# Kernel optimization log

Measured on AMD Instinct MI355X. Metric: run time of the kernel, lower is better.

The kernel has to match this reference:

```python
import jax, jax.numpy as jnp
import numpy as np

N_DOC, N_WORD, N_ENT, N_POS = 10000, 20000, 10000, 60
D, D_POS_IN, D_WEMB = 128, 60, 300
E11, E22, E33, E01, E02, E03 = 320000, 160000, 3600, 300000, 100000, 150000
EPS = 1e-9


def spmm(rows, cols, vals, x, n_out):
    """Sparse (n_out x n_in) adjacency @ x via gather + weighted segment-sum."""
    return jax.ops.segment_sum(vals[:, None] * x[cols], rows, num_segments=n_out)


def gcn(rows, cols, vals, x, n_out, W=None, b=None):
    """GCN layer: adj @ (x W + b) with ReLU; identity=True in torch == W is None."""
    h = x if W is None else x @ W + b
    return jax.nn.relu(spmm(rows, cols, vals, h, n_out))


def setup_inputs():
    key = jax.random.key(0)
    ks = iter(jax.random.split(key, 64))
    randn = lambda s: jax.random.normal(next(ks), s, jnp.float32)
    rand = lambda s: jax.random.uniform(next(ks), s, dtype=jnp.float32)
    ridx = lambda s, hi: jax.random.randint(next(ks), s, 0, hi, jnp.int32)
    return {
        "f1": randn((N_WORD, D)),
        "f2": randn((N_ENT, D)),
        "f3": randn((N_POS, D_POS_IN)),
        "word_emb": randn((N_ENT, D_WEMB)),
        "a11_rows": ridx((E11,), N_WORD), "a11_cols": ridx((E11,), N_WORD), "a11_vals": rand((E11,)),
        "a22_rows": ridx((E22,), N_ENT), "a22_cols": ridx((E22,), N_ENT), "a22_vals": rand((E22,)),
        "a33_rows": ridx((E33,), N_POS), "a33_cols": ridx((E33,), N_POS), "a33_vals": rand((E33,)),
        "a01_rows": ridx((E01,), N_DOC), "a01_cols": ridx((E01,), N_WORD), "a01_vals": rand((E01,)),
        "a02_rows": ridx((E02,), N_DOC), "a02_cols": ridx((E02,), N_ENT), "a02_vals": rand((E02,)),
        "a03_rows": ridx((E03,), N_DOC), "a03_cols": ridx((E03,), N_POS), "a03_vals": rand((E03,)),
        "W3": randn((D_POS_IN, D)) * 0.1, "b3": jnp.zeros((D,), jnp.float32),
        "W1_2": randn((D, D)) * 0.1, "b1_2": jnp.zeros((D,), jnp.float32),
        "W2_2": randn((D, D)) * 0.1, "b2_2": jnp.zeros((D,), jnp.float32),
        "W3_2": randn((D, D)) * 0.1, "b3_2": jnp.zeros((D,), jnp.float32),
    }


def reference(f1, f2, f3, word_emb,
              a11_rows, a11_cols, a11_vals, a22_rows, a22_cols, a22_vals,
              a33_rows, a33_cols, a33_vals, a01_rows, a01_cols, a01_vals,
              a02_rows, a02_cols, a02_vals, a03_rows, a03_cols, a03_vals,
              W3, b3, W1_2, b1_2, W2_2, b2_2, W3_2, b3_2):
    # eval mode: F.dropout(training=False) is a no-op
    # type 1 (words): GCN(identity=True) -> GCN_2
    h1 = gcn(a11_rows, a11_cols, a11_vals, f1, N_WORD)
    h1 = gcn(a11_rows, a11_cols, a11_vals, h1, N_WORD, W1_2, b1_2)
    # type 2 (entities, concat_word_emb=True): GCN(identity=True) -> GCN_2 -> concat word_emb
    h2 = gcn(a22_rows, a22_cols, a22_vals, f2, N_ENT)
    h2 = gcn(a22_rows, a22_cols, a22_vals, h2, N_ENT, W2_2, b2_2)
    h2 = jnp.concatenate([h2, word_emb], axis=-1)  # [N_ENT, D + D_WEMB]
    # type 3 (POS): full GCN -> GCN_2
    h3 = gcn(a33_rows, a33_cols, a33_vals, f3, N_POS, W3, b3)
    h3 = gcn(a33_rows, a33_cols, a33_vals, h3, N_POS, W3_2, b3_2)
    # cross-type aggregation onto documents + L2 normalization
    outs = []
    for rows, cols, vals, h in ((a01_rows, a01_cols, a01_vals, h1),
                                (a02_rows, a02_cols, a02_vals, h2),
                                (a03_rows, a03_cols, a03_vals, h3)):
        agg = spmm(rows, cols, vals, h, N_DOC)  # [N_DOC, d]
        outs.append(agg / (jnp.linalg.norm(agg, axis=-1, keepdims=True) + EPS))
    return tuple(outs)
```

## Files before the change

kernel.cpp:

```cpp
#include <hip/hip_runtime.h>
#include <hip/hip_bf16.h>

typedef __hip_bfloat16 bf16;

#define N_DOC   10000
#define N_WORD  20000
#define N_ENT   10000
#define N_POS   60
#define DD      128
#define D_WEMB  300
#define E11     320000
#define E22     160000
#define E33     3600
#define E01     300000
#define E02     100000
#define E03     150000

#define ROFF11  0
#define ROFF22  20000
#define ROFF33  30000
#define ROFF01  30060
#define ROFF02  40060
#define ROFF03  50060
#define NROWS   60060
#define EOFF11  0
#define EOFF22  320000
#define EOFF33  480000
#define EOFF01  483600
#define EOFF02  783600
#define EOFF03  883600
#define NEDGES  1033600

#define BSHIFT  9
#define NBUCK   118
#define BCAP    18432
#define P1_TILE 4096
#define P1_EPT  8

__device__ __forceinline__ float loadf(const void* p, size_t i, int isb) {
    return isb ? __bfloat162float(((const bf16*)p)[i])
               : ((const float*)p)[i];
}
__device__ __forceinline__ float b2f(unsigned u16) {
    union { unsigned v; float f; } x; x.v = u16 << 16; return x.f;
}
__device__ __forceinline__ unsigned f2b(float f) {
    bf16 h = __float2bfloat16(f);
    union { bf16 h; unsigned short u; } x; x.h = h; return (unsigned)x.u;
}
__device__ __forceinline__ void storef(void* p, size_t i, int asb, float v) {
    if (asb) ((unsigned short*)p)[i] = (unsigned short)f2b(v);
    else     ((float*)p)[i] = v;
}
__device__ __forceinline__ unsigned pack_pair(int col, float v) {
    return (f2b(v) << 16) | (unsigned)col;
}

__device__ __forceinline__ void edge_decode(
        int i,
        const int* __restrict__ r11, const int* __restrict__ c11, const void* __restrict__ v11,
        const int* __restrict__ r22, const int* __restrict__ c22, const void* __restrict__ v22,
        const int* __restrict__ r33, const int* __restrict__ c33, const void* __restrict__ v33,
        const int* __restrict__ r01, const int* __restrict__ c01, const void* __restrict__ v01,
        const int* __restrict__ r02, const int* __restrict__ c02, const void* __restrict__ v02,
        const int* __restrict__ r03, const int* __restrict__ c03, const void* __restrict__ v03,
        int isb, int& slot, int& col, float& val) {
    if      (i < EOFF22) { int k = i;          slot = ROFF11 + r11[k]; col = c11[k]; val = loadf(v11, k, isb); }
    else if (i < EOFF33) { int k = i - EOFF22; slot = ROFF22 + r22[k]; col = c22[k]; val = loadf(v22, k, isb); }
    else if (i < EOFF01) { int k = i - EOFF33; slot = ROFF33 + r33[k]; col = c33[k]; val = loadf(v33, k, isb); }
    else if (i < EOFF02) { int k = i - EOFF01; slot = ROFF01 + r01[k]; col = c01[k]; val = loadf(v01, k, isb); }
    else if (i < EOFF03) { int k = i - EOFF02; slot = ROFF02 + r02[k]; col = c02[k]; val = loadf(v02, k, isb); }
    else                 { int k = i - EOFF03; slot = ROFF03 + r03[k]; col = c03[k]; val = loadf(v03, k, isb); }
}

__global__ void detect_kernel(const unsigned* __restrict__ probe, int* __restrict__ flag,
                              int* __restrict__ bcur) {
    __shared__ int cnt;
    if (threadIdx.x == 0) cnt = 0;
    __syncthreads();
    int insane = 0;
    for (int i = threadIdx.x; i < 1024; i += 256) {
        float x = __uint_as_float(probe[i]);
        float a = fabsf(x);
        if (!(a > 1e-10f && a < 1e10f)) insane++;
    }
    atomicAdd(&cnt, insane);
    if (bcur && threadIdx.x < NBUCK) bcur[threadIdx.x] = threadIdx.x * BCAP;
    __syncthreads();
    if (threadIdx.x == 0) *flag = (cnt > 512) ? 1 : 0;
}

__global__ __launch_bounds__(512) void bin_edges(
        const int* __restrict__ r11, const int* __restrict__ c11, const void* __restrict__ v11,
        const int* __restrict__ r22, const int* __restrict__ c22, const void* __restrict__ v22,
        const int* __restrict__ r33, const int* __restrict__ c33, const void* __restrict__ v33,
        const int* __restrict__ r01, const int* __restrict__ c01, const void* __restrict__ v01,
        const int* __restrict__ r02, const int* __restrict__ c02, const void* __restrict__ v02,
        const int* __restrict__ r03, const int* __restrict__ c03, const void* __restrict__ v03,
        int* __restrict__ bcur, uint2* __restrict__ staging,
        const int* __restrict__ dflag) {
    __shared__ int hist[NBUCK], gbase[NBUCK], cursor[NBUCK];
    int t = threadIdx.x;
    if (t < NBUCK) { hist[t] = 0; cursor[t] = 0; }
    __syncthreads();
    int isb = *dflag;
    int base0 = blockIdx.x * P1_TILE;
    unsigned rx[P1_EPT], ry[P1_EPT];
    int bk[P1_EPT];
    #pragma unroll
    for (int k = 0; k < P1_EPT; ++k) {
        int i = base0 + t + k * 512;
        bk[k] = -1;
        if (i < NEDGES) {
            int slot, col; float val;
            edge_decode(i, r11, c11, v11, r22, c22, v22, r33, c33, v33,
                        r01, c01, v01, r02, c02, v02, r03, c03, v03,
                        isb, slot, col, val);
            rx[k] = ((unsigned)slot << 16) | (unsigned)col;
            ry[k] = f2b(val);
            bk[k] = slot >> BSHIFT;
            atomicAdd(&hist[bk[k]], 1);
        }
    }
    __syncthreads();
    if (t < NBUCK) {
        int c = hist[t];
        gbase[t] = c ? atomicAdd(bcur + t, c) : 0;
    }
    __syncthreads();
    #pragma unroll
    for (int k = 0; k < P1_EPT; ++k) {
        if (bk[k] >= 0) {
            int p = atomicAdd(&cursor[bk[k]], 1);
            int dst = gbase[bk[k]] + p;
            if (dst < (bk[k] + 1) * BCAP)
                staging[dst] = make_uint2(rx[k], ry[k]);
        }
    }
}

__global__ void scan_buckets(const int* __restrict__ bcur, int* __restrict__ bbase,
                             int* __restrict__ G) {
    __shared__ int wtop[2];
    int t = threadIdx.x;
    int cnt = 0;
    if (t < NBUCK) {
        int c = bcur[t] - t * BCAP;
        cnt = (c < BCAP) ? c : BCAP;
    }
    int lane = t & 63, w = t >> 6;
    int s = cnt;
    #pragma unroll
    for (int off = 1; off < 64; off <<= 1) {
        int y = __shfl_up(s, off);
        if (lane >= off) s += y;
    }
    if (lane == 63) wtop[w] = s;
    __syncthreads();
    int woff = (w > 0) ? wtop[0] : 0;
    if (t < NBUCK) bbase[t] = woff + s - cnt;
    if (t == NBUCK - 1) { bbase[NBUCK] = woff + s; G[NROWS] = woff + s; }
}

__global__ __launch_bounds__(512) void finalize_csr(
        const int* __restrict__ bcur, const int* __restrict__ bbase,
        const uint2* __restrict__ staging,
        int* __restrict__ G, unsigned* __restrict__ pairs) {
    __shared__ int h[512], rp[512], cu[512];
    __shared__ int wsum2[8];
    int b = blockIdx.x, t = threadIdx.x;
    int cnt = bcur[b] - b * BCAP;
    if (cnt > BCAP) cnt = BCAP;
    int bb = bbase[b];
    h[t] = 0;
    __syncthreads();
    const uint2* st = staging + (size_t)b * BCAP;
    for (int i = t; i < cnt; i += 512)
        atomicAdd(&h[(st[i].x >> 16) & 511], 1);
    __syncthreads();
    int lane = t & 63, w = t >> 6;
    int x = h[t];
    int s = x;
    #pragma unroll
    for (int off = 1; off < 64; off <<= 1) {
        int y = __shfl_up(s, off);
        if (lane >= off) s += y;
    }
    if (lane == 63) wsum2[w] = s;
    __syncthreads();
    if (t < 8) {
        int v = wsum2[t];
        #pragma unroll
        for (int off = 1; off < 8; off <<= 1) {
            int y = __shfl_up(v, off);
            if (lane >= off) v += y;
        }
        wsum2[t] = v;
    }
    __syncthreads();
    int myrp = ((w > 0) ? wsum2[w - 1] : 0) + s - x;
    rp[t] = myrp;
    cu[t] = 0;
    int slot = (b << BSHIFT) + t;
    if (slot < NROWS) G[slot] = bb + myrp;
    __syncthreads();
    for (int i = t; i < cnt; i += 512) {
        uint2 r = st[i];
        int sl = (r.x >> 16) & 511;
        int p = atomicAdd(&cu[sl], 1);
        pairs[bb + rp[sl] + p] = (r.y << 16) | (r.x & 0xffffu);
    }
}

__global__ void hist2_kernel(const int* __restrict__ rowsA, int nEA,
                             const int* __restrict__ rowsB, int nEB,
                             int nA, int* __restrict__ cnt) {
    int i = blockIdx.x * blockDim.x + threadIdx.x;
    if (i < nEA) atomicAdd(cnt + rowsA[i], 1);
    else if (i < nEA + nEB) atomicAdd(cnt + nA + rowsB[i - nEA], 1);
}

__device__ void scan_ex(const int* __restrict__ cnt, int* __restrict__ rp, int n) {
    __shared__ int wsum[16];
    __shared__ int carry;
    int t = threadIdx.x, lane = t & 63, w = t >> 6;
    if (t == 0) carry = 0;
    __syncthreads();
    for (int base = 0; base < n; base += 1024) {
        int i = base + t;
        int x = (i < n) ? cnt[i] : 0;
        int s = x;
        #pragma unroll
        for (int off = 1; off < 64; off <<= 1) {
            int y = __shfl_up(s, off);
            if (lane >= off) s += y;
        }
        if (lane == 63) wsum[w] = s;
        __syncthreads();
        if (w == 0) {
            int v = (lane < 16) ? wsum[lane] : 0;
            #pragma unroll
            for (int off = 1; off < 16; off <<= 1) {
// ... 225 lines not shown
            unsigned u0 = ((const unsigned*)((const bf16*)src1 + (size_t)c0 * DD))[lane];
            unsigned u1 = ((const unsigned*)((const bf16*)src1 + (size_t)c1 * DD))[lane];
            x0 = b2f(u0 & 0xffffu); x1 = b2f(u0 >> 16);
            y0 = b2f(u1 & 0xffffu); y1 = b2f(u1 >> 16);
        } else {
            float2 x = ((const float2*)((const float*)src1 + (size_t)c0 * DD))[lane];
            float2 y = ((const float2*)((const float*)src1 + (size_t)c1 * DD))[lane];
            x0 = x.x; x1 = x.y; y0 = y.x; y1 = y.y;
        }
        x0 = fmaxf(x0, 0.f); x1 = fmaxf(x1, 0.f);
        y0 = fmaxf(y0, 0.f); y1 = fmaxf(y1, 0.f);
        a1.x = fmaf(v0, x0, a1.x); a1.y = fmaf(v0, x1, a1.y);
        b1.x = fmaf(v1, y0, b1.x); b1.y = fmaf(v1, y1, b1.y);
        if (s2b) {
            const unsigned* s0p = (const unsigned*)((const bf16*)src2 + (size_t)c0 * D_WEMB);
            const unsigned* s1p = (const unsigned*)((const bf16*)src2 + (size_t)c1 * D_WEMB);
            #pragma unroll
            for (int s = 0; s < 3; ++s) {
                int pi = lane + 64 * s;
                if (pi < P2) {
                    unsigned u0 = s0p[pi], u1 = s1p[pi];
                    a2[s].x  = fmaf(v0, b2f(u0 & 0xffffu), a2[s].x);
                    a2[s].y  = fmaf(v0, b2f(u0 >> 16),     a2[s].y);
                    b2v[s].x = fmaf(v1, b2f(u1 & 0xffffu), b2v[s].x);
                    b2v[s].y = fmaf(v1, b2f(u1 >> 16),     b2v[s].y);
                }
            }
        } else {
            const float2* s0p = (const float2*)((const float*)src2 + (size_t)c0 * D_WEMB);
            const float2* s1p = (const float2*)((const float*)src2 + (size_t)c1 * D_WEMB);
            #pragma unroll
            for (int s = 0; s < 3; ++s) {
                int pi = lane + 64 * s;
                if (pi < P2) {
                    float2 x = s0p[pi], y = s1p[pi];
                    a2[s].x  = fmaf(v0, x.x, a2[s].x);
                    a2[s].y  = fmaf(v0, x.y, a2[s].y);
                    b2v[s].x = fmaf(v1, y.x, b2v[s].x);
                    b2v[s].y = fmaf(v1, y.y, b2v[s].y);
                }
            }
        }
    }
    if (e < e1) {
        unsigned pp = pairs[e];
        int c = pp & 0xffffu;
        float v = b2f(pp >> 16);
        float x0, x1;
        if (s1b) {
            unsigned u = ((const unsigned*)((const bf16*)src1 + (size_t)c * DD))[lane];
            x0 = b2f(u & 0xffffu); x1 = b2f(u >> 16);
        } else {
            float2 x = ((const float2*)((const float*)src1 + (size_t)c * DD))[lane];
            x0 = x.x; x1 = x.y;
        }
        x0 = fmaxf(x0, 0.f); x1 = fmaxf(x1, 0.f);
        a1.x = fmaf(v, x0, a1.x); a1.y = fmaf(v, x1, a1.y);
        if (s2b) {
            const unsigned* sp = (const unsigned*)((const bf16*)src2 + (size_t)c * D_WEMB);
            #pragma unroll
            for (int s = 0; s < 3; ++s) {
                int pi = lane + 64 * s;
                if (pi < P2) {
                    unsigned u = sp[pi];
                    a2[s].x = fmaf(v, b2f(u & 0xffffu), a2[s].x);
                    a2[s].y = fmaf(v, b2f(u >> 16),     a2[s].y);
                }
            }
        } else {
            const float2* sp = (const float2*)((const float*)src2 + (size_t)c * D_WEMB);
            #pragma unroll
            for (int s = 0; s < 3; ++s) {
                int pi = lane + 64 * s;
                if (pi < P2) {
                    float2 x = sp[pi];
                    a2[s].x = fmaf(v, x.x, a2[s].x);
                    a2[s].y = fmaf(v, x.y, a2[s].y);
                }
            }
        }
    }
    float t1x = a1.x + b1.x, t1y = a1.y + b1.y;
    float t2x[3], t2y[3];
    #pragma unroll
    for (int s = 0; s < 3; ++s) { t2x[s] = a2[s].x + b2v[s].x; t2y[s] = a2[s].y + b2v[s].y; }
    float ss = t1x * t1x + t1y * t1y;
    #pragma unroll
    for (int s = 0; s < 3; ++s) {
        int pi = lane + 64 * s;
        if (pi < P2) ss += t2x[s] * t2x[s] + t2y[s] * t2y[s];
    }
    #pragma unroll
    for (int off = 32; off > 0; off >>= 1) ss += __shfl_down(ss, off);
    ss = __shfl(ss, 0);
    float inv = 1.0f / (sqrtf(ss) + 1e-9f);
    size_t base = elem_off + (size_t)row * (DD + D_WEMB);
    if (isb) {
        ((unsigned*)((bf16*)out + base))[lane] = f2b(t1x * inv) | (f2b(t1y * inv) << 16);
        unsigned* o2 = (unsigned*)((bf16*)out + base + DD);
        #pragma unroll
        for (int s = 0; s < 3; ++s) {
            int pi = lane + 64 * s;
            if (pi < P2) o2[pi] = f2b(t2x[s] * inv) | (f2b(t2y[s] * inv) << 16);
        }
    } else {
        ((float2*)((float*)out + base))[lane] = make_float2(t1x * inv, t1y * inv);
        float2* o2 = (float2*)((float*)out + base + DD);
        #pragma unroll
        for (int s = 0; s < 3; ++s) {
            int pi = lane + 64 * s;
            if (pi < P2) o2[pi] = make_float2(t2x[s] * inv, t2y[s] * inv);
        }
    }
}

template<bool RELU, int K>
__device__ __forceinline__ void rowpar_body256(
        const void* __restrict__ X, int xisb,
        const void* __restrict__ W, const void* __restrict__ b,
        void* __restrict__ out, int oisb, int isb,
        int row, int tid, float* xr ) {
    int half = tid >> 7;
    int j = tid & 127;
    float* xrh = xr + half * K;
    if (j < K) {
        float x = loadf(X, (size_t)row * K + j, xisb);
        if (RELU) x = fmaxf(x, 0.f);
        xrh[j] = x;
    }
    __syncthreads();
    float acc = loadf(b, j, isb);
    #pragma unroll 8
    for (int k = 0; k < K; ++k)
        acc = fmaf(xrh[k], loadf(W, (size_t)k * 128 + j, isb), acc);
    storef(out, (size_t)row * 128 + j, oisb, acc);
}

template<bool RELU>
__global__ void spmm_gather128(const int* __restrict__ rowptr, const unsigned* __restrict__ pairs,
                               const void* __restrict__ src, int src_flagged,
                               void* __restrict__ dst, int dst_flagged,
                               int n, const int* __restrict__ dflag) {
    int row = blockIdx.x * 4 + (threadIdx.x >> 6);
    if (row >= n) return;
    int isb = *dflag;
    gather128_body<RELU>(rowptr, pairs, src, src_flagged ? isb : 0,
                         dst, dst_flagged ? isb : 0, row, threadIdx.x & 63);
}

template<int KP, bool PRELU>
__global__ void hop_pos(const int* __restrict__ G, const unsigned* __restrict__ pairs,
                        int roff1, const void* __restrict__ src1, void* __restrict__ dst1, int n1, int B1,
                        int roff2, const void* __restrict__ src2, void* __restrict__ dst2, int n2, int B2,
                        int src_flagged, int dst_flagged,
                        const void* __restrict__ PX, const void* __restrict__ PW,
                        const void* __restrict__ Pb, void* __restrict__ PO,
                        const int* __restrict__ dflag) {
    __shared__ float xr[2 * KP];
    int isb = *dflag;
    int b = blockIdx.x;
    if (b < B1) {
        int row = b * 4 + (threadIdx.x >> 6);
        if (row >= n1) return;
        gather128_body<false>(G + roff1, pairs, src1, src_flagged ? isb : 0,
                              dst1, dst_flagged ? isb : 0, row, threadIdx.x & 63);
    } else if (b < B1 + B2) {
        int row = (b - B1) * 4 + (threadIdx.x >> 6);
        if (row >= n2) return;
        gather128_body<false>(G + roff2, pairs, src2, src_flagged ? isb : 0,
                              dst2, dst_flagged ? isb : 0, row, threadIdx.x & 63);
    } else {
        int row = (b - B1 - B2) * 2 + (threadIdx.x >> 7);
        if (row >= N_POS) return;
        rowpar_body256<PRELU, KP>(PX, isb, PW, Pb, PO, isb, isb, row, threadIdx.x, xr);
    }
}

template<bool RELU>
__global__ void spmm_norm128(const int* __restrict__ rowptr, const unsigned* __restrict__ pairs,
                             const void* __restrict__ src, int src_flagged,
                             void* __restrict__ out, size_t elem_off,
                             int n, const int* __restrict__ dflag) {
    int row = blockIdx.x * 4 + (threadIdx.x >> 6);
    if (row >= n) return;
    int isb = *dflag;
    norm128_body<RELU>(rowptr, pairs, src, src_flagged ? isb : 0, out, elem_off,
                       row, threadIdx.x & 63, isb);
}

__global__ void spmm2_norm(const int* __restrict__ rowptr, const unsigned* __restrict__ pairs,
                           const void* __restrict__ src1, int s1_flagged,
                           const void* __restrict__ src2, int s2_flagged,
                           void* __restrict__ out, size_t elem_off,
                           int n, const int* __restrict__ dflag) {
    int row = blockIdx.x * 4 + (threadIdx.x >> 6);
    if (row >= n) return;
    int isb = *dflag;
    norm428_body(rowptr, pairs, src1, s1_flagged ? isb : 0, src2, s2_flagged ? isb : 0,
                 out, elem_off, row, threadIdx.x & 63, isb);
}

__global__ void final_norm_all(const int* __restrict__ G, const unsigned* __restrict__ pairs,
                               const void* __restrict__ s1, const void* __restrict__ e0b,
                               const void* __restrict__ wemb, const void* __restrict__ p3b,
                               void* __restrict__ out,
                               size_t off1, size_t off2, size_t off3,
                               const int* __restrict__ dflag) {
    int isb = *dflag;
    int lane = threadIdx.x & 63;
    int b = blockIdx.x;
    if (b < 2500) {
        int row = b * 4 + (threadIdx.x >> 6);
        if (row >= N_DOC) return;
        norm128_body<true>(G + ROFF01, pairs, s1, isb, out, off1, row, lane, isb);
    } else if (b < 5000) {
        int row = (b - 2500) * 4 + (threadIdx.x >> 6);
        if (row >= N_DOC) return;
        norm428_body(G + ROFF02, pairs, e0b, isb, wemb, isb, out, off2, row, lane, isb);
    } else {
        int row = (b - 5000) * 4 + (threadIdx.x >> 6);
        if (row >= N_DOC) return;
        norm128_body<true>(G + ROFF03, pairs, p3b, isb, out, off3, row, lane, isb);
    }
}

template<bool RELU>
__global__ void spmm_kernel(const int* __restrict__ rows, const int* __restrict__ cols,
                            const void* __restrict__ vals,
                            const void* __restrict__ src, int sstride, int src_flagged,
                            float* __restrict__ dst, int dstride, int doff,
                            int d, int nE, const int* __restrict__ dflag) {
    int e = blockIdx.x * (blockDim.x >> 6) + (threadIdx.x >> 6);
    if (e >= nE) return;
    int isb  = *dflag;
    int sisb = src_flagged ? isb : 0;
    int lane = threadIdx.x & 63;
    int r = rows[e];
    int c = cols[e];
    float v = loadf(vals, e, isb);
    size_t sbase = (size_t)c * sstride;
    float* dp = dst + (size_t)r * dstride + doff;
    if (sisb) {
        const unsigned* sp = (const unsigned*)((const bf16*)src + sbase);
        for (int j = 2 * lane; j < d; j += 128) {
            unsigned u = sp[j >> 1];
            float x0 = b2f(u & 0xffffu);
            float x1 = b2f(u >> 16);
            if (RELU) { x0 = fmaxf(x0, 0.f); x1 = fmaxf(x1, 0.f); }
            atomicAdd(dp + j,     v * x0);
            atomicAdd(dp + j + 1, v * x1);
        }
    } else {
        const float2* sp = (const float2*)((const float*)src + sbase);
        for (int j = 2 * lane; j < d; j += 128) {
            float2 x = sp[j >> 1];
            if (RELU) { x.x = fmaxf(x.x, 0.f); x.y = fmaxf(x.y, 0.f); }
            atomicAdd(dp + j,     v * x.x);
            atomicAdd(dp + j + 1, v * x.y);
        }
    }
}

template<bool RELU>
__device__ __forceinline__ void gemm_tile_body(
        const float* __restrict__ X, const void* __restrict__ W,
        const void* __restrict__ b, void* __restrict__ out, int n,
        int bx, int by, int isb, float* Wl ) {
    if (bx * 64 >= n) return;
    int tid = threadIdx.x;
    int jc = by * 64;
    if (isb) {
        const uint2* Wg = (const uint2*)W;
        float4* Wl4 = (float4*)Wl;
        for (int vidx = tid; vidx < 2048; vidx += 256) {
            int k = vidx >> 4, jl4 = vidx & 15;
            uint2 u = Wg[k * 32 + (jc >> 2) + jl4];
            float4 vv;
            vv.x = b2f(u.x & 0xffffu);
            vv.y = b2f(u.x >> 16);
            vv.z = b2f(u.y & 0xffffu);
            vv.w = b2f(u.y >> 16);
            Wl4[vidx] = vv;
        }
    } else {
        const float4* Wg = (const float4*)W;
        float4* Wl4 = (float4*)Wl;
        for (int vidx = tid; vidx < 2048; vidx += 256) {
            int k = vidx >> 4, jl4 = vidx & 15;
            Wl4[vidx] = Wg[k * 32 + (jc >> 2) + jl4];
        }
    }
    __syncthreads();
    int j2 = tid & 31;
    int g  = tid >> 5;
    float bc0 = loadf(b, jc + 2 * j2, isb);
    float bc1 = loadf(b, jc + 2 * j2 + 1, isb);
    int i0 = bx * 64 + g * 8;
    float a0[8], a1[8];
    #pragma unroll
    for (int r = 0; r < 8; ++r) { a0[r] = bc0; a1[r] = bc1; }
    const float4* xp = (const float4*)(X + (size_t)i0 * 128);
    const float2* Wl2 = (const float2*)Wl;
    #pragma unroll 2
    for (int k4 = 0; k4 < 32; ++k4) {
        float2 w0 = Wl2[(4 * k4 + 0) * 32 + j2];
        float2 w1 = Wl2[(4 * k4 + 1) * 32 + j2];
        float2 w2 = Wl2[(4 * k4 + 2) * 32 + j2];
        float2 w3 = Wl2[(4 * k4 + 3) * 32 + j2];
        #pragma unroll
        for (int r = 0; r < 8; ++r) {
            float4 v = xp[r * 32 + k4];
            if (RELU) {
                v.x = fmaxf(v.x, 0.f); v.y = fmaxf(v.y, 0.f);
                v.z = fmaxf(v.z, 0.f); v.w = fmaxf(v.w, 0.f);
            }
            a0[r] = fmaf(v.w, w3.x, fmaf(v.z, w2.x, fmaf(v.y, w1.x, fmaf(v.x, w0.x, a0[r]))));
            a1[r] = fmaf(v.w, w3.y, fmaf(v.z, w2.y, fmaf(v.y, w1.y, fmaf(v.x, w0.y, a1[r]))));
        }
    }
    #pragma unroll
    for (int r = 0; r < 8; ++r) {
        int i = i0 + r;
        if (i < n) {
            if (isb) {
                ((unsigned*)((bf16*)out + (size_t)i * 128 + jc))[j2] =
                    f2b(a0[r]) | (f2b(a1[r]) << 16);
            } else {
                ((float2*)((float*)out + (size_t)i * 128 + jc))[j2] =
                    make_float2(a0[r], a1[r]);
            }
        }
    }
}

template<bool RELU>
__global__ __launch_bounds__(256) void gemm_tile(
        const float* __restrict__ X, const void* __restrict__ W,
        const void* __restrict__ b, void* __restrict__ out, int n,
        const int* __restrict__ dflag) {
    __shared__ float Wl[128 * 64];
    gemm_tile_body<RELU>(X, W, b, out, n, blockIdx.x, blockIdx.y, *dflag, Wl);
}

template<bool RELU>
__global__ __launch_bounds__(256) void gemm_tile_b2g(
        const float* __restrict__ X1, const void* __restrict__ W1, const void* __restrict__ b1,
        void* __restrict__ out1, int n1, int G1,
        const float* __restrict__ X2, const void* __restrict__ W2, const void* __restrict__ b2,
        void* __restrict__ out2, int n2, int GT,
        const int* __restrict__ G33, const unsigned* __restrict__ pairs,
        const void* __restrict__ P3a, void* __restrict__ P3b,
        const int* __restrict__ dflag) {
    __shared__ float Wl[128 * 64];
    int isb = *dflag;
    int x = blockIdx.x;
    if (x < G1) {
        gemm_tile_body<RELU>(X1, W1, b1, out1, n1, x, blockIdx.y, isb, Wl);
    } else if (x < GT) {
        gemm_tile_body<RELU>(X2, W2, b2, out2, n2, x - G1, blockIdx.y, isb, Wl);
    } else {
        if (blockIdx.y != 0) return;
        int row = (x - GT) * 4 + (threadIdx.x >> 6);
        if (row >= N_POS) return;
        gather128_body<false>(G33, pairs, P3a, isb, P3b, isb, row, threadIdx.x & 63);
    }
}

template<bool RELU>
__global__ __launch_bounds__(256) void gemm128_kernel(
        const float* __restrict__ X, const void* __restrict__ W,
        const void* __restrict__ b, float* __restrict__ out, int n,
        const int* __restrict__ dflag) {
    __shared__ float Wl[128 * 128];
    int isb = *dflag;
    int tid = threadIdx.x;
    if (isb) {
        const uint2* Wg = (const uint2*)W;
        float4* Wl4 = (float4*)Wl;
        for (int idx = tid; idx < 4096; idx += 256) {
            uint2 u = Wg[idx];
            float4 vv;
            vv.x = b2f(u.x & 0xffffu);
            vv.y = b2f(u.x >> 16);
            vv.z = b2f(u.y & 0xffffu);
            vv.w = b2f(u.y >> 16);
            Wl4[idx] = vv;
        }
    } else {
        const float4* Wg = (const float4*)W;
        float4* Wl4 = (float4*)Wl;
        for (int idx = tid; idx < 4096; idx += 256) Wl4[idx] = Wg[idx];
    }
    __syncthreads();
    int j = tid & 127;
    int h = tid >> 7;
    float bj = loadf(b, j, isb);
    int row0 = blockIdx.x * 64 + h * 32;
    for (int q = 0; q < 8; ++q) {
        int gi = row0 + q * 4;
        if (gi >= n) break;
        const float4* x0 = (const float4*)(X + (size_t)gi * 128);
        const float4* x1 = x0 + 32;
        const float4* x2 = x1 + 32;
        const float4* x3 = x2 + 32;
        float a0 = bj, a1 = bj, a2 = bj, a3 = bj;
        #pragma unroll 4
        for (int k4 = 0; k4 < 32; ++k4) {
            float4 v0 = x0[k4], v1 = x1[k4], v2 = x2[k4], v3 = x3[k4];
            if (RELU) {
                v0.x = fmaxf(v0.x, 0.f); v0.y = fmaxf(v0.y, 0.f); v0.z = fmaxf(v0.z, 0.f); v0.w = fmaxf(v0.w, 0.f);
                v1.x = fmaxf(v1.x, 0.f); v1.y = fmaxf(v1.y, 0.f); v1.z = fmaxf(v1.z, 0.f); v1.w = fmaxf(v1.w, 0.f);
                v2.x = fmaxf(v2.x, 0.f); v2.y = fmaxf(v2.y, 0.f); v2.z = fmaxf(v2.z, 0.f); v2.w = fmaxf(v2.w, 0.f);
                v3.x = fmaxf(v3.x, 0.f); v3.y = fmaxf(v3.y, 0.f); v3.z = fmaxf(v3.z, 0.f); v3.w = fmaxf(v3.w, 0.f);
            }
            float w0 = Wl[(4 * k4 + 0) * 128 + j];
            float w1 = Wl[(4 * k4 + 1) * 128 + j];
            float w2 = Wl[(4 * k4 + 2) * 128 + j];
            float w3 = Wl[(4 * k4 + 3) * 128 + j];
            a0 = fmaf(v0.w, w3, fmaf(v0.z, w2, fmaf(v0.y, w1, fmaf(v0.x, w0, a0))));
            a1 = fmaf(v1.w, w3, fmaf(v1.z, w2, fmaf(v1.y, w1, fmaf(v1.x, w0, a1))));
            a2 = fmaf(v2.w, w3, fmaf(v2.z, w2, fmaf(v2.y, w1, fmaf(v2.x, w0, a2))));
            a3 = fmaf(v3.w, w3, fmaf(v3.z, w2, fmaf(v3.y, w1, fmaf(v3.x, w0, a3))));
        }
        float* o = out + (size_t)gi * 128 + j;
        o[0] = a0; o[128] = a1; o[256] = a2; o[384] = a3;
    }
}

template<bool RELU, int K>
__global__ void rowpar_gemm(const void* __restrict__ X, int x_flagged,
                            const void* __restrict__ W, const void* __restrict__ b,
                            void* __restrict__ out, int out_flagged,
                            const int* __restrict__ dflag) {
    __shared__ float xr[K];
    int isb  = *dflag;
    int xisb = x_flagged ? isb : 0;
    int oisb = out_flagged ? isb : 0;
    int row = blockIdx.x;
    int j = threadIdx.x;
    if (j < K) {
        float x = loadf(X, (size_t)row * K + j, xisb);
        if (RELU) x = fmaxf(x, 0.f);
        xr[j] = x;
    }
    __syncthreads();
    float acc = loadf(b, j, isb);
    #pragma unroll 8
    for (int k = 0; k < K; ++k)
        acc = fmaf(xr[k], loadf(W, (size_t)k * 128 + j, isb), acc);
    storef(out, (size_t)row * 128 + j, oisb, acc);
}

template<bool RELU, int K>
__global__ void gemm_kernel(const void* __restrict__ X, int x_flagged,
                            const void* __restrict__ W,
                            const void* __restrict__ b,
                            float* __restrict__ out, int n,
                            const int* __restrict__ dflag) {
    __shared__ float Wl[K * 128];
    int isb  = *dflag;
    int xisb = x_flagged ? isb : 0;
    int j = threadIdx.x;
    for (int idx = j; idx < K * 128; idx += 128)
        Wl[idx] = loadf(W, idx, isb);
    __syncthreads();
    float bj = loadf(b, j, isb);
    int row0 = blockIdx.x * 64;
    for (int i0 = 0; i0 < 64; i0 += 4) {
        int i = row0 + i0;
        if (i >= n) break;
        size_t r0 = (size_t)i * K;
        float a0 = bj, a1 = bj, a2 = bj, a3 = bj;
        for (int k = 0; k < K; ++k) {
            float w = Wl[k * 128 + j];
            float v0 = loadf(X, r0 + k, xisb);
            float v1 = loadf(X, r0 + K + k, xisb);
            float v2 = loadf(X, r0 + 2 * K + k, xisb);
            float v3 = loadf(X, r0 + 3 * K + k, xisb);
            if (RELU) {
                v0 = fmaxf(v0, 0.f); v1 = fmaxf(v1, 0.f);
                v2 = fmaxf(v2, 0.f); v3 = fmaxf(v3, 0.f);
            }
            a0 = fmaf(v0, w, a0);
            a1 = fmaf(v1, w, a1);
            a2 = fmaf(v2, w, a2);
            a3 = fmaf(v3, w, a3);
        }
        float* o = out + (size_t)i * 128 + j;
        o[0] = a0; o[128] = a1; o[256] = a2; o[384] = a3;
    }
}

__global__ void l2norm_kernel(const float* __restrict__ agg, int d,
                              void* __restrict__ out, size_t elem_off, int n,
                              const int* __restrict__ dflag) {
    int row = blockIdx.x * (blockDim.x >> 6) + (threadIdx.x >> 6);
    if (row >= n) return;
    int isb  = *dflag;
    int lane = threadIdx.x & 63;
    const float2* a2 = (const float2*)(agg + (size_t)row * d);
    float ss = 0.f;
    for (int j = 2 * lane; j < d; j += 128) {
        float2 x = a2[j >> 1];
        ss += x.x * x.x + x.y * x.y;
    }
    #pragma unroll
    for (int off = 32; off > 0; off >>= 1) ss += __shfl_down(ss, off);
    ss = __shfl(ss, 0);
    float inv = 1.0f / (sqrtf(ss) + 1e-9f);
    size_t bbase = elem_off + (size_t)row * d;
    if (isb) {
        unsigned* o = (unsigned*)((bf16*)out + bbase);
        for (int j = 2 * lane; j < d; j += 128) {
            float2 x = a2[j >> 1];
            o[j >> 1] = f2b(x.x * inv) | (f2b(x.y * inv) << 16);
        }
    } else {
        float2* o = (float2*)((float*)out + bbase);
        for (int j = 2 * lane; j < d; j += 128) {
            float2 x = a2[j >> 1];
            o[j >> 1] = make_float2(x.x * inv, x.y * inv);
        }
    }
}

static inline int spmm_grid(int nE) { return (nE + 3) / 4; }
static inline int row_grid(int n)   { return (n + 3) / 4; }
static inline int pad8(int x)       { return (x + 7) & ~7; }

static void build2(hipStream_t stream,
                   const int* rowsA, const int* colsA, const void* valsA, int nA, int nEA,
                   const int* rowsB, const int* colsB, const void* valsB, int nB, int nEB,
                   int* rpA, int* rpB, int* curAB, unsigned* pairsA, unsigned* pairsB,
                   const int* dflag) {
    int nE = nEA + nEB;
    hipMemsetAsync(curAB, 0, (size_t)(nA + nB) * 4, stream);
    hist2_kernel<<<(nE + 255) / 256, 256, 0, stream>>>(rowsA, nEA, rowsB, nEB, nA, curAB);
    scan2_kernel<<<1, 1024, 0, stream>>>(curAB, rpA, nA, curAB + nA, rpB, nB);
    copy2_kernel<<<(nA + nB + 255) / 256, 256, 0, stream>>>(rpA, rpB, nA, nB, curAB);
    scatter2_kernel<<<(nE + 255) / 256, 256, 0, stream>>>(
        rowsA, colsA, valsA, nEA, rowsB, colsB, valsB, nEB, nA, curAB, pairsA, pairsB, dflag);
}

extern "C" void kernel_launch(void* const* d_in, const int* in_sizes, int n_in,
                              void* d_out, int out_size, void* d_ws, size_t ws_size,
                              hipStream_t stream) {
    const void* f1   = d_in[0];
    const void* f2   = d_in[1];
    const void* f3   = d_in[2];
    const void* wemb = d_in[3];
    const int*  a11r = (const int*)d_in[4];
    const int*  a11c = (const int*)d_in[5];
    const void* a11v = d_in[6];
    const int*  a22r = (const int*)d_in[7];
    const int*  a22c = (const int*)d_in[8];
    const void* a22v = d_in[9];
    const int*  a33r = (const int*)d_in[10];
    const int*  a33c = (const int*)d_in[11];
    const void* a33v = d_in[12];
    const int*  a01r = (const int*)d_in[13];
    const int*  a01c = (const int*)d_in[14];
    const void* a01v = d_in[15];
    const int*  a02r = (const int*)d_in[16];
    const int*  a02c = (const int*)d_in[17];
    const void* a02v = d_in[18];
    const int*  a03r = (const int*)d_in[19];
    const int*  a03c = (const int*)d_in[20];
    const void* a03v = d_in[21];
    const void* W3   = d_in[22];
    const void* b3   = d_in[23];
    const void* W1_2 = d_in[24];
    const void* b1_2 = d_in[25];
    const void* W2_2 = d_in[26];
    const void* b2_2 = d_in[27];
    const void* W3_2 = d_in[28];
    const void* b3_2 = d_in[29];

    int*   dflag = (int*)d_ws;
    float* base  = (float*)d_ws + 16;

    const size_t OUT1_OFF = 0;
    const size_t OUT2_OFF = (size_t)N_DOC * DD;
    const size_t OUT3_OFF = OUT2_OFF + (size_t)N_DOC * (DD + D_WEMB);

    dim3 blk(256);

    const size_t BF_S0 = 0, BF_S1 = 2560000, BF_E0 = 5120000, BF_E1 = 6400000;
    const size_t BF_P3A = 7680000, BF_P3B = 7687680, BF_INT = 7695360;
    const size_t BIG_INTS = (size_t)(NROWS + 1) + NROWS + 128 + NEDGES + 8;
    const size_t WS_BIG = 64 + (BF_INT + BIG_INTS) * 4;
    const size_t WS_MID = 64 + 22240000ull + (60008ull + 620000ull) * 4;

    if (ws_size >= WS_BIG) {
        float* S0  = base + BF_S0;
        float* S1  = base + BF_S1;
        float* E0  = base + BF_E0;
        float* E1  = base + BF_E1;
        float* P3a = base + BF_P3A;
        float* P3b = base + BF_P3B;
        int*   G     = (int*)(base + BF_INT);
        int*   bcur  = G + (NROWS + 1);
        int*   bbase = bcur + 128;
        unsigned* pairs = (unsigned*)(bbase + 132);
        uint2* staging = (uint2*)base;

        detect_kernel<<<1, 256, 0, stream>>>((const unsigned*)f1, dflag, bcur);

        const int NB1 = (NEDGES + P1_TILE - 1) / P1_TILE;
        bin_edges<<<NB1, 512, 0, stream>>>(
            a11r, a11c, a11v, a22r, a22c, a22v, a33r, a33c, a33v,
            a01r, a01c, a01v, a02r, a02c, a02v, a03r, a03c, a03v,
            bcur, staging, dflag);
        scan_buckets<<<1, 128, 0, stream>>>(bcur, bbase, G);
        finalize_csr<<<NBUCK, 512, 0, stream>>>(bcur, bbase, staging, G, pairs);

        int B1 = row_grid(N_WORD), B2 = row_grid(N_ENT);
        hop_pos<60, false><<<B1 + B2 + 30, blk, 0, stream>>>(
            G, pairs, ROFF11, f1, S0, N_WORD, B1,
            ROFF22, f2, E0, N_ENT, B2, 1, 0,
            f3, W3, b3, P3a, dflag);
        {
            int G1 = pad8((N_WORD + 63) / 64), G2 = pad8((N_ENT + 63) / 64);
            int GT = G1 + G2;
            gemm_tile_b2g<true><<<dim3(GT + row_grid(N_POS), 2), 256, 0, stream>>>(
                S0, W1_2, b1_2, S1, N_WORD, G1,
                E0, W2_2, b2_2, E1, N_ENT, GT,
                G + ROFF33, pairs, P3a, P3b, dflag);
        }
        hop_pos<128, true><<<B1 + B2 + 30, blk, 0, stream>>>(
            G, pairs, ROFF11, S1, S0, N_WORD, B1,
            ROFF22, E1, E0, N_ENT, B2, 1, 1,
            P3b, W3_2, b3_2, P3a, dflag);
        spmm_gather128<false><<<row_grid(N_POS), blk, 0, stream>>>(
            G + ROFF33, pairs, P3a, 1, P3b, 1, N_POS, dflag);

        final_norm_all<<<7500, blk, 0, stream>>>(
            G, pairs, S0, E0, wemb, P3b, d_out, OUT1_OFF, OUT2_OFF, OUT3_OFF, dflag);
    } else if (ws_size >= WS_MID) {
        detect_kernel<<<1, 256, 0, stream>>>((const unsigned*)f1, dflag, (int*)nullptr);
        float* S0   = base;
        float* S1   = base + 2560000;
        float* E0   = base;
        float* E1   = base + 1280000;
        float* P3a  = base;
        float* P3b  = base + 7680;
        int* I = (int*)(base + 5560000);
        {
            int* rpA = I; int* rpB = rpA + (N_WORD + 1); int* cur = rpB + (N_DOC + 1);
            unsigned* pA = (unsigned*)(cur + N_WORD + N_DOC); unsigned* pB = pA + E11;
            build2(stream, a11r, a11c, a11v, N_WORD, E11,
                   a01r, a01c, a01v, N_DOC, E01, rpA, rpB, cur, pA, pB, dflag);
            spmm_gather128<false><<<row_grid(N_WORD), blk, 0, stream>>>(
                rpA, pA, f1, 1, S0, 0, N_WORD, dflag);
            gemm_tile<true><<<dim3(pad8((N_WORD + 63) / 64), 2), 256, 0, stream>>>(
                S0, W1_2, b1_2, S1, N_WORD, dflag);
            spmm_gather128<false><<<row_grid(N_WORD), blk, 0, stream>>>(
                rpA, pA, S1, 1, S0, 1, N_WORD, dflag);
            spmm_norm128<true><<<row_grid(N_DOC), blk, 0, stream>>>(
                rpB, pB, S0, 1, d_out, OUT1_OFF, N_DOC, dflag);
        }
        {
            int* rpA = I; int* rpB = rpA + (N_ENT + 1); int* cur = rpB + (N_DOC + 1);
            unsigned* pA = (unsigned*)(cur + N_ENT + N_DOC); unsigned* pB = pA + E22;
            build2(stream, a22r, a22c, a22v, N_ENT, E22,
                   a02r, a02c, a02v, N_DOC, E02, rpA, rpB, cur, pA, pB, dflag);
            spmm_gather128<false><<<row_grid(N_ENT), blk, 0, stream>>>(
                rpA, pA, f2, 1, E0, 0, N_ENT, dflag);
            gemm_tile<true><<<dim3(pad8((N_ENT + 63) / 64), 2), 256, 0, stream>>>(
                E0, W2_2, b2_2, E1, N_ENT, dflag);
            spmm_gather128<false><<<row_grid(N_ENT), blk, 0, stream>>>(
                rpA, pA, E1, 1, E0, 1, N_ENT, dflag);
            spmm2_norm<<<row_grid(N_DOC), blk, 0, stream>>>(
                rpB, pB, E0, 1, wemb, 1, d_out, OUT2_OFF, N_DOC, dflag);
        }
        {
            int* rpA = I; int* rpB = rpA + (N_POS + 1); int* cur = rpB + (N_DOC + 1);
            unsigned* pA = (unsigned*)(cur + N_POS + N_DOC); unsigned* pB = pA + E33;
            build2(stream, a33r, a33c, a33v, N_POS, E33,
                   a03r, a03c, a03v, N_DOC, E03, rpA, rpB, cur, pA, pB, dflag);
            rowpar_gemm<false, 60><<<N_POS, 128, 0, stream>>>(
                f3, 1, W3, b3, P3a, 1, dflag);
            spmm_gather128<false><<<row_grid(N_POS), blk, 0, stream>>>(
                rpA, pA, P3a, 1, P3b, 1, N_POS, dflag);
            rowpar_gemm<true, 128><<<N_POS, 128, 0, stream>>>(
                P3b, 1, W3_2, b3_2, P3a, 1, dflag);
            spmm_gather128<false><<<row_grid(N_POS), blk, 0, stream>>>(
                rpA, pA, P3a, 1, P3b, 1, N_POS, dflag);
            spmm_norm128<true><<<row_grid(N_DOC), blk, 0, stream>>>(
                rpB, pB, P3b, 1, d_out, OUT3_OFF, N_DOC, dflag);
        }
    } else {
        detect_kernel<<<1, 256, 0, stream>>>((const unsigned*)f1, dflag, (int*)nullptr);
        float* S0   = base;
        float* S1   = base + 2560000;
        float* AGG1 = S1;
        float* E0   = base;
        float* E1   = base + 1280000;
        float* AGG2 = base + 1280000;
        float* P3a  = base;
        float* P3b  = base + 7680;
        float* AGG3 = base + 15360;
        hipMemsetAsync(S0, 0, (size_t)N_WORD * DD * 4, stream);
        spmm_kernel<false><<<spmm_grid(E11), blk, 0, stream>>>(
            a11r, a11c, a11v, f1, DD, 1, S0, DD, 0, DD, E11, dflag);
        gemm128_kernel<true><<<(N_WORD + 63) / 64, 256, 0, stream>>>(
            S0, W1_2, b1_2, S1, N_WORD, dflag);
        hipMemsetAsync(S0, 0, (size_t)N_WORD * DD * 4, stream);
        spmm_kernel<false><<<spmm_grid(E11), blk, 0, stream>>>(
            a11r, a11c, a11v, S1, DD, 0, S0, DD, 0, DD, E11, dflag);
        hipMemsetAsync(AGG1, 0, (size_t)N_DOC * DD * 4, stream);
        spmm_kernel<true><<<spmm_grid(E01), blk, 0, stream>>>(
            a01r, a01c, a01v, S0, DD, 0, AGG1, DD, 0, DD, E01, dflag);
        l2norm_kernel<<<row_grid(N_DOC), blk, 0, stream>>>(
            AGG1, DD, d_out, OUT1_OFF, N_DOC, dflag);

        hipMemsetAsync(E0, 0, (size_t)N_ENT * DD * 4, stream);
        spmm_kernel<false><<<spmm_grid(E22), blk, 0, stream>>>(
            a22r, a22c, a22v, f2, DD, 1, E0, DD, 0, DD, E22, dflag);
        gemm128_kernel<true><<<(N_ENT + 63) / 64, 256, 0, stream>>>(
            E0, W2_2, b2_2, E1, N_ENT, dflag);
        hipMemsetAsync(E0, 0, (size_t)N_ENT * DD * 4, stream);
        spmm_kernel<false><<<spmm_grid(E22), blk, 0, stream>>>(
            a22r, a22c, a22v, E1, DD, 0, E0, DD, 0, DD, E22, dflag);
        hipMemsetAsync(AGG2, 0, (size_t)N_DOC * (DD + D_WEMB) * 4, stream);
        spmm_kernel<true><<<spmm_grid(E02), blk, 0, stream>>>(
            a02r, a02c, a02v, E0, DD, 0, AGG2, DD + D_WEMB, 0, DD, E02, dflag);
        spmm_kernel<false><<<spmm_grid(E02), blk, 0, stream>>>(
            a02r, a02c, a02v, wemb, D_WEMB, 1, AGG2, DD + D_WEMB, DD, D_WEMB, E02, dflag);
        l2norm_kernel<<<row_grid(N_DOC), blk, 0, stream>>>(
            AGG2, DD + D_WEMB, d_out, OUT2_OFF, N_DOC, dflag);

        gemm_kernel<false, 60><<<1, 128, 0, stream>>>(f3, 1, W3, b3, P3a, N_POS, dflag);
        hipMemsetAsync(P3b, 0, (size_t)N_POS * DD * 4, stream);
        spmm_kernel<false><<<spmm_grid(E33), blk, 0, stream>>>(
            a33r, a33c, a33v, P3a, DD, 0, P3b, DD, 0, DD, E33, dflag);
        gemm128_kernel<true><<<1, 256, 0, stream>>>(
            P3b, W3_2, b3_2, P3a, N_POS, dflag);
        hipMemsetAsync(P3b, 0, (size_t)N_POS * DD * 4, stream);
        spmm_kernel<false><<<spmm_grid(E33), blk, 0, stream>>>(
            a33r, a33c, a33v, P3a, DD, 0, P3b, DD, 0, DD, E33, dflag);
        hipMemsetAsync(AGG3, 0, (size_t)N_DOC * DD * 4, stream);
        spmm_kernel<true><<<spmm_grid(E03), blk, 0, stream>>>(
            a03r, a03c, a03v, P3b, DD, 0, AGG3, DD, 0, DD, E03, dflag);
        l2norm_kernel<<<row_grid(N_DOC), blk, 0, stream>>>(
            AGG3, DD, d_out, OUT3_OFF, N_DOC, dflag);
    }
}
```

Before: 323.4 us.

## Convert inputs to bf16 upfront and keep all intermediates in bf16

```diff
diff --git a/kernel.cpp b/kernel.cpp
--- a/kernel.cpp
+++ b/kernel.cpp
@@ -36,6 +36,17 @@
 #define BCAP    18432
 #define P1_TILE 4096
 #define P1_EPT  8
+
+#define BFO_F1B     0
+#define BFO_F2B     1280000
+#define BFO_WEMBB   1920000
+#define BFO_E0B     3420000
+#define BFO_S0B     4349952
+#define BFO_S1B     5629952
+#define BFO_E1B     6909952
+#define BFO_P3A     7549952
+#define BFO_P3B     7557632
+#define BFO_INT     7565312
 
 __device__ __forceinline__ float loadf(const void* p, size_t i, int isb) {
     return isb ? __bfloat162float(((const bf16*)p)[i])
@@ -88,6 +99,33 @@
     if (bcur && threadIdx.x < NBUCK) bcur[threadIdx.x] = threadIdx.x * BCAP;
     __syncthreads();
     if (threadIdx.x == 0) *flag = (cnt > 512) ? 1 : 0;
+}
+
+__device__ __forceinline__ void conv_seg(const void* __restrict__ src,
+                                         unsigned* __restrict__ dst,
+                                         int npairs, int isb, int tid, int stride) {
+    if (isb) {
+        const unsigned* s = (const unsigned*)src;
+        for (int i = tid; i < npairs; i += stride) dst[i] = s[i];
+    } else {
+        const float2* s = (const float2*)src;
+        for (int i = tid; i < npairs; i += stride) {
+            float2 x = s[i];
+            dst[i] = f2b(x.x) | (f2b(x.y) << 16);
+        }
+    }
+}
+__global__ void convert_bf16(const void* __restrict__ f1, const void* __restrict__ f2,
+                             const void* __restrict__ wemb,
+                             unsigned* __restrict__ f1b, unsigned* __restrict__ f2b,
+                             unsigned* __restrict__ wembB,
+                             const int* __restrict__ dflag) {
+    int isb = *dflag;
+    int tid = blockIdx.x * blockDim.x + threadIdx.x;
+    int stride = gridDim.x * blockDim.x;
+    conv_seg(f1,   f1b,   N_WORD * (DD / 2),     isb, tid, stride);
+    conv_seg(f2,   f2b,   N_ENT  * (DD / 2),     isb, tid, stride);
+    conv_seg(wemb, wembB, N_ENT  * (D_WEMB / 2), isb, tid, stride);
 }
 
 __global__ __launch_bounds__(512) void bin_edges(
@@ -619,24 +657,21 @@
 __global__ void hop_pos(const int* __restrict__ G, const unsigned* __restrict__ pairs,
                         int roff1, const void* __restrict__ src1, void* __restrict__ dst1, int n1, int B1,
                         int roff2, const void* __restrict__ src2, void* __restrict__ dst2, int n2, int B2,
-                        int src_flagged, int dst_flagged,
                         const void* __restrict__ PX, const void* __restrict__ PW,
                         const void* __restrict__ Pb, void* __restrict__ PO,
                         const int* __restrict__ dflag) {
     __shared__ float xr[2 * KP];
-    int isb = *dflag;
     int b = blockIdx.x;
     if (b < B1) {
         int row = b * 4 + (threadIdx.x >> 6);
         if (row >= n1) return;
-        gather128_body<false>(G + roff1, pairs, src1, src_flagged ? isb : 0,
-                              dst1, dst_flagged ? isb : 0, row, threadIdx.x & 63);
+        gather128_body<false>(G + roff1, pairs, src1, 1, dst1, 1, row, threadIdx.x & 63);
     } else if (b < B1 + B2) {
         int row = (b - B1) * 4 + (threadIdx.x >> 6);
         if (row >= n2) return;
-        gather128_body<false>(G + roff2, pairs, src2, src_flagged ? isb : 0,
-                              dst2, dst_flagged ? isb : 0, row, threadIdx.x & 63);
+        gather128_body<false>(G + roff2, pairs, src2, 1, dst2, 1, row, threadIdx.x & 63);
     } else {
+        int isb = *dflag;
         int row = (b - B1 - B2) * 2 + (threadIdx.x >> 7);
         if (row >= N_POS) return;
         rowpar_body256<PRELU, KP>(PX, isb, PW, Pb, PO, isb, isb, row, threadIdx.x, xr);
@@ -679,11 +714,11 @@
     if (b < 2500) {
         int row = b * 4 + (threadIdx.x >> 6);
         if (row >= N_DOC) return;
-        norm128_body<true>(G + ROFF01, pairs, s1, isb, out, off1, row, lane, isb);
+        norm128_body<true>(G + ROFF01, pairs, s1, 1, out, off1, row, lane, isb);
     } else if (b < 5000) {
         int row = (b - 2500) * 4 + (threadIdx.x >> 6);
         if (row >= N_DOC) return;
-        norm428_body(G + ROFF02, pairs, e0b, isb, wemb, isb, out, off2, row, lane, isb);
+        norm428_body(G + ROFF02, pairs, e0b, 1, wemb, 1, out, off2, row, lane, isb);
     } else {
         int row = (b - 5000) * 4 + (threadIdx.x >> 6);
         if (row >= N_DOC) return;
@@ -728,11 +763,11 @@
     }
 }
 
-template<bool RELU>
+template<bool RELU, bool XB>
 __device__ __forceinline__ void gemm_tile_body(
-        const float* __restrict__ X, const void* __restrict__ W,
+        const void* __restrict__ X, const void* __restrict__ W,
         const void* __restrict__ b, void* __restrict__ out, int n,
-        int bx, int by, int isb, float* Wl ) {
+        int bx, int by, int isb, int oisb, float* Wl ) {
     if (bx * 64 >= n) return;
     int tid = threadIdx.x;
     int jc = by * 64;
@@ -766,7 +801,7 @@
     float a0[8], a1[8];
     #pragma unroll
     for (int r = 0; r < 8; ++r) { a0[r] = bc0; a1[r] = bc1; }
-    const float4* xp = (const float4*)(X + (size_t)i0 * 128);
+    const char* xbase = (const char*)X + (size_t)i0 * 128 * (XB ? 2 : 4);
     const float2* Wl2 = (const float2*)Wl;
     #pragma unroll 2
     for (int k4 = 0; k4 < 32; ++k4) {
@@ -776,7 +811,14 @@
         float2 w3 = Wl2[(4 * k4 + 3) * 32 + j2];
         #pragma unroll
         for (int r = 0; r < 8; ++r) {
-            float4 v = xp[r * 32 + k4];
+            float4 v;
+            if (XB) {
+                uint2 u = ((const uint2*)xbase)[r * 32 + k4];
+                v.x = b2f(u.x & 0xffffu); v.y = b2f(u.x >> 16);
+                v.z = b2f(u.y & 0xffffu); v.w = b2f(u.y >> 16);
+            } else {
+                v = ((const float4*)xbase)[r * 32 + k4];
+            }
             if (RELU) {
                 v.x = fmaxf(v.x, 0.f); v.y = fmaxf(v.y, 0.f);
                 v.z = fmaxf(v.z, 0.f); v.w = fmaxf(v.w, 0.f);
@@ -789,7 +831,7 @@
     for (int r = 0; r < 8; ++r) {
         int i = i0 + r;
         if (i < n) {
-            if (isb) {
+            if (oisb) {
                 ((unsigned*)((bf16*)out + (size_t)i * 128 + jc))[j2] =
                     f2b(a0[r]) | (f2b(a1[r]) << 16);
             } else {
@@ -806,14 +848,15 @@
         const void* __restrict__ b, void* __restrict__ out, int n,
         const int* __restrict__ dflag) {
     __shared__ float Wl[128 * 64];
-    gemm_tile_body<RELU>(X, W, b, out, n, blockIdx.x, blockIdx.y, *dflag, Wl);
+    int isb = *dflag;
+    gemm_tile_body<RELU, false>(X, W, b, out, n, blockIdx.x, blockIdx.y, isb, isb, Wl);
 }
 
 template<bool RELU>
 __global__ __launch_bounds__(256) void gemm_tile_b2g(
-        const float* __restrict__ X1, const void* __restrict__ W1, const void* __restrict__ b1,
+        const void* __restrict__ X1, const void* __restrict__ W1, const void* __restrict__ b1,
         void* __restrict__ out1, int n1, int G1,
-        const float* __restrict__ X2, const void* __restrict__ W2, const void* __restrict__ b2,
+        const void* __restrict__ X2, const void* __restrict__ W2, const void* __restrict__ b2,
         void* __restrict__ out2, int n2, int GT,
         const int* __restrict__ G33, const unsigned* __restrict__ pairs,
         const void* __restrict__ P3a, void* __restrict__ P3b,
@@ -822,9 +865,9 @@
     int isb = *dflag;
     int x = blockIdx.x;
     if (x < G1) {
-        gemm_tile_body<RELU>(X1, W1, b1, out1, n1, x, blockIdx.y, isb, Wl);
+        gemm_tile_body<RELU, true>(X1, W1, b1, out1, n1, x, blockIdx.y, isb, 1, Wl);
     } else if (x < GT) {
-        gemm_tile_body<RELU>(X2, W2, b2, out2, n2, x - G1, blockIdx.y, isb, Wl);
+        gemm_tile_body<RELU, true>(X2, W2, b2, out2, n2, x - G1, blockIdx.y, isb, 1, Wl);
     } else {
         if (blockIdx.y != 0) return;
         int row = (x - GT) * 4 + (threadIdx.x >> 6);
@@ -1052,24 +1095,25 @@
 
     dim3 blk(256);
 
-    const size_t BF_S0 = 0, BF_S1 = 2560000, BF_E0 = 5120000, BF_E1 = 6400000;
-    const size_t BF_P3A = 7680000, BF_P3B = 7687680, BF_INT = 7695360;
-    const size_t BIG_INTS = (size_t)(NROWS + 1) + NROWS + 128 + NEDGES + 8;
-    const size_t WS_BIG = 64 + (BF_INT + BIG_INTS) * 4;
+    const size_t BIG_INTS = (size_t)(NROWS + 1) + 128 + 132 + NEDGES;
+    const size_t WS_BIG = 64 + ((size_t)BFO_INT + BIG_INTS) * 4;
     const size_t WS_MID = 64 + 22240000ull + (60008ull + 620000ull) * 4;
 
     if (ws_size >= WS_BIG) {
-        float* S0  = base + BF_S0;
-        float* S1  = base + BF_S1;
-        float* E0  = base + BF_E0;
-        float* E1  = base + BF_E1;
-        float* P3a = base + BF_P3A;
-        float* P3b = base + BF_P3B;
-        int*   G     = (int*)(base + BF_INT);
+        uint2* staging = (uint2*)base;
+        void*  f1b   = (void*)(base + BFO_F1B);
+        void*  f2b   = (void*)(base + BFO_F2B);
+        void*  wembB = (void*)(base + BFO_WEMBB);
+        void*  E0b   = (void*)(base + BFO_E0B);
+        void*  S0b   = (void*)(base + BFO_S0B);
+        void*  S1b   = (void*)(base + BFO_S1B);
+        void*  E1b   = (void*)(base + BFO_E1B);
+        float* P3a   = base + BFO_P3A;
+        float* P3b   = base + BFO_P3B;
+        int*   G     = (int*)(base + BFO_INT);
         int*   bcur  = G + (NROWS + 1);
         int*   bbase = bcur + 128;
         unsigned* pairs = (unsigned*)(bbase + 132);
-        uint2* staging = (uint2*)base;
 
         detect_kernel<<<1, 256, 0, stream>>>((const unsigned*)f1, dflag, bcur);
 
@@ -1081,28 +1125,31 @@
         scan_buckets<<<1, 128, 0, stream>>>(bcur, bbase, G);
         finalize_csr<<<NBUCK, 512, 0, stream>>>(bcur, bbase, staging, G, pairs);
 
+        convert_bf16<<<2048, 256, 0, stream>>>(
+            f1, f2, wemb, (unsigned*)f1b, (unsigned*)f2b, (unsigned*)wembB, dflag);
+
         int B1 = row_grid(N_WORD), B2 = row_grid(N_ENT);
         hop_pos<60, false><<<B1 + B2 + 30, blk, 0, stream>>>(
-            G, pairs, ROFF11, f1, S0, N_WORD, B1,
-            ROFF22, f2, E0, N_ENT, B2, 1, 0,
+            G, pairs, ROFF11, f1b, S0b, N_WORD, B1,
+            ROFF22, f2b, E0b, N_ENT, B2,
             f3, W3, b3, P3a, dflag);
         {
             int G1 = pad8((N_WORD + 63) / 64), G2 = pad8((N_ENT + 63) / 64);
             int GT = G1 + G2;
             gemm_tile_b2g<true><<<dim3(GT + row_grid(N_POS), 2), 256, 0, stream>>>(
-                S0, W1_2, b1_2, S1, N_WORD, G1,
-                E0, W2_2, b2_2, E1, N_ENT, GT,
+                S0b, W1_2, b1_2, S1b, N_WORD, G1,
+                E0b, W2_2, b2_2, E1b, N_ENT, GT,
                 G + ROFF33, pairs, P3a, P3b, dflag);
         }
         hop_pos<128, true><<<B1 + B2 + 30, blk, 0, stream>>>(
-            G, pairs, ROFF11, S1, S0, N_WORD, B1,
-            ROFF22, E1, E0, N_ENT, B2, 1, 1,
+            G, pairs, ROFF11, S1b, S0b, N_WORD, B1,
+            ROFF22, E1b, E0b, N_ENT, B2,
             P3b, W3_2, b3_2, P3a, dflag);
         spmm_gather128<false><<<row_grid(N_POS), blk, 0, stream>>>(
             G + ROFF33, pairs, P3a, 1, P3b, 1, N_POS, dflag);
 
         final_norm_all<<<7500, blk, 0, stream>>>(
-            G, pairs, S0, E0, wemb, P3b, d_out, OUT1_OFF, OUT2_OFF, OUT3_OFF, dflag);
+            G, pairs, S0b, E0b, wembB, P3b, d_out, OUT1_OFF, OUT2_OFF, OUT3_OFF, dflag);
     } else if (ws_size >= WS_MID) {
         detect_kernel<<<1, 256, 0, stream>>>((const unsigned*)f1, dflag, (int*)nullptr);
         float* S0   = base;
```

New measurement: 294.2 us. 9.1% less time.
